# Kernel optimization log

Hardware: AMD Instinct MI355X
Metric: run time of the kernel (lower is better)

The kernel has to match this reference:

```python
import jax, jax.numpy as jnp
import numpy as np


def _shared_mlp(x, W, s, b):
    # 1x1 conv over channel dim (last axis) + folded BN (scale/shift) + ReLU
    # x: (..., Cin), W: (Cout, Cin), s/b: (Cout,)
    return jax.nn.relu(jnp.einsum('...c,oc->...o', x, W) * s + b)


def setup_inputs() -> dict:
    key = jax.random.key(0)
    ks = jax.random.split(key, 15)
    B, N, K, C = 4, 4096, 32, 64
    D1, D2, DH = 64, 64, 128
    sc = 0.1
    return {
        'xyz': jax.random.normal(ks[0], (B, N, 3), dtype=jnp.float32),
        'features': jax.random.normal(ks[1], (B, C, N), dtype=jnp.float32),
        'idx': jax.random.randint(ks[2], (N, K), 0, N, dtype=jnp.int32),
        'W_gu': jax.random.normal(ks[3], (D1, 6), dtype=jnp.float32) * sc,
        's_gu': jnp.ones((D1,), jnp.float32),
        'b_gu': jax.random.normal(ks[4], (D1,), dtype=jnp.float32) * sc,
        'W_gv': jax.random.normal(ks[5], (D2, C), dtype=jnp.float32) * sc,
        's_gv': jnp.ones((D2,), jnp.float32),
        'b_gv': jax.random.normal(ks[6], (D2,), dtype=jnp.float32) * sc,
        'W_h': jax.random.normal(ks[7], (DH, D1 + D2), dtype=jnp.float32) * sc,
        's_h': jnp.ones((DH,), jnp.float32),
        'b_h': jax.random.normal(ks[8], (DH,), dtype=jnp.float32) * sc,
        'W_f': jax.random.normal(ks[9], (C, DH), dtype=jnp.float32) * sc,
        's_f': jnp.ones((C,), jnp.float32),
        'b_f': jax.random.normal(ks[10], (C,), dtype=jnp.float32) * sc,
    }


def reference(xyz, features, idx, W_gu, s_gu, b_gu, W_gv, s_gv, b_gv,
              W_h, s_h, b_h, W_f, s_f, b_f):
    # xyz: (B,N,3), features: (B,C,N), idx: (N,K) neighbor indices per point
    feats = jnp.swapaxes(features, 1, 2)              # (B,N,C)
    xyz_nb = xyz[:, idx, :]                           # (B,N,K,3) random gather
    feat_nb = feats[:, idx, :]                        # (B,N,K,C)
    K = idx.shape[1]
    center_xyz = jnp.broadcast_to(xyz[:, :, None, :], xyz_nb.shape)
    rel_xyz = jnp.concatenate([center_xyz, xyz_nb], axis=-1)   # (B,N,K,6)
    rel_feat = feat_nb + feats[:, :, None, :]                  # (B,N,K,C)

    gu = _shared_mlp(rel_xyz, W_gu, s_gu, b_gu)       # (B,N,K,D1)
    gv = _shared_mlp(rel_feat, W_gv, s_gv, b_gv)      # (B,N,K,D2)
    fuse = jnp.concatenate([gu, gv], axis=-1)         # (B,N,K,D1+D2)
    h = _shared_mlp(fuse, W_h, s_h, b_h)              # (B,N,K,DH)
    pooled = jnp.mean(h, axis=2)                      # (B,N,DH) mean over K
    out = _shared_mlp(pooled, W_f, s_f, b_f)          # (B,N,C)
    out = jnp.swapaxes(out, 1, 2) + features          # (B,C,N) residual
    return (xyz, out)
```

## Files before the change

kernel.cpp:

```cpp
#include <hip/hip_runtime.h>

#define B_  4
#define N_  4096
#define K_  32
#define C_  64
#define DH_ 128
#define PPB 16

typedef _Float16 half2v __attribute__((ext_vector_type(2)));
typedef _Float16 half8  __attribute__((ext_vector_type(8)));
typedef __fp16   fp16x2 __attribute__((ext_vector_type(2)));
typedef float  floatx16 __attribute__((ext_vector_type(16)));
typedef unsigned int uint_t;

union HU { half2v h; uint_t u; };
union HU2 { fp16x2 h; uint_t u; };

__device__ __forceinline__ uint_t pk2(float a, float b) {
    HU2 x; x.h = __builtin_amdgcn_cvt_pkrtz(a, b);
    return x.u;
}

__global__ __launch_bounds__(256) void k_prep(
    const float* __restrict__ xyz,
    const float* __restrict__ features,
    const float* __restrict__ W_gv,
    const float* __restrict__ W_gu,
    const float* __restrict__ s_gu, const float* __restrict__ b_gu,
    const float* __restrict__ s_gv, const float* __restrict__ b_gv,
    const float* __restrict__ W_h,  const float* __restrict__ s_h,
    float* __restrict__ out_xyz,
    _Float16* __restrict__ Bpack,
    uint_t* __restrict__ QsH,
    uint_t* __restrict__ PcatH)
{
    const int blk = blockIdx.x;
    const int b   = blk >> 7;
    const int n0  = (blk & 127) * 32;
    const int t   = threadIdx.x;

    if (t < 96) { int e = blk*96 + t; out_xyz[e] = xyz[e]; }
    {
        int e = blk*32 + t;
        if (t < 32) {
            int j = e & 7, l = (e >> 3) & 63, c = (e >> 9) & 7, ob = e >> 12;
            int o = ob*32 + (l & 31);
            int i = c*16 + (l >> 5)*8 + j;
            Bpack[e] = (_Float16)(W_h[o*DH_ + i] * s_h[o]);
        }
    }

    __shared__ __align__(16) float ftile[64 * 33];
    __shared__ __align__(16) float wtile[64 * 68];

#pragma unroll
    for (int r = 0; r < 2; r++) {
        const int i4 = r*256 + t, c = i4 >> 3, nq = i4 & 7;
        const float4 f4 = *(const float4*)&features[(b*C_ + c)*N_ + n0 + nq*4];
        ftile[c*33 + nq*4 + 0] = f4.x;
        ftile[c*33 + nq*4 + 1] = f4.y;
        ftile[c*33 + nq*4 + 2] = f4.z;
        ftile[c*33 + nq*4 + 3] = f4.w;
    }
#pragma unroll
    for (int r = 0; r < 4; r++) {
        const int e4 = r*256 + t, o = e4 >> 4, c0 = (e4 & 15)*4;
        const float4 w4 = *(const float4*)&W_gv[o*C_ + c0];
        wtile[(c0+0)*68 + o] = w4.x;
        wtile[(c0+1)*68 + o] = w4.y;
        wtile[(c0+2)*68 + o] = w4.z;
        wtile[(c0+3)*68 + o] = w4.w;
    }
    __syncthreads();

    const int n  = t >> 3;
    const int og = t & 7;
    const int o0 = og * 8;

    float acc[8] = {};
    for (int c = 0; c < 64; c++) {
        const float a = ftile[c*33 + n];
        float wv[8];
        *(float4*)&wv[0] = *(const float4*)&wtile[c*68 + o0];
        *(float4*)&wv[4] = *(const float4*)&wtile[c*68 + o0 + 4];
#pragma unroll
        for (int oo = 0; oo < 8; oo++)
            acc[oo] = fmaf(a, wv[oo], acc[oo]);
    }

    const int bn = b*N_ + n0 + n;
    const float x0 = xyz[bn*3+0], x1 = xyz[bn*3+1], x2 = xyz[bn*3+2];

    float sgu[8], bgu[8], sgv[8], bgv[8];
    *(float4*)&sgu[0] = *(const float4*)&s_gu[o0]; *(float4*)&sgu[4] = *(const float4*)&s_gu[o0+4];
    *(float4*)&bgu[0] = *(const float4*)&b_gu[o0]; *(float4*)&bgu[4] = *(const float4*)&b_gu[o0+4];
    *(float4*)&sgv[0] = *(const float4*)&s_gv[o0]; *(float4*)&sgv[4] = *(const float4*)&s_gv[o0+4];
    *(float4*)&bgv[0] = *(const float4*)&b_gv[o0]; *(float4*)&bgv[4] = *(const float4*)&b_gv[o0+4];

    float qv[8], rv[8];
#pragma unroll
    for (int oo = 0; oo < 8; oo++) {
        const int o = o0 + oo;
        qv[oo] = x0*W_gu[o*6+0] + x1*W_gu[o*6+1] + x2*W_gu[o*6+2];
        rv[oo] = x0*W_gu[o*6+3] + x1*W_gu[o*6+4] + x2*W_gu[o*6+5];
    }
    uint4 qa, pa;
    qa.x = pk2(qv[0]*sgu[0]+bgu[0], qv[1]*sgu[1]+bgu[1]);
    qa.y = pk2(qv[2]*sgu[2]+bgu[2], qv[3]*sgu[3]+bgu[3]);
    qa.z = pk2(qv[4]*sgu[4]+bgu[4], qv[5]*sgu[5]+bgu[5]);
    qa.w = pk2(qv[6]*sgu[6]+bgu[6], qv[7]*sgu[7]+bgu[7]);
    pa.x = pk2(rv[0]*sgu[0], rv[1]*sgu[1]);
    pa.y = pk2(rv[2]*sgu[2], rv[3]*sgu[3]);
    pa.z = pk2(rv[4]*sgu[4], rv[5]*sgu[5]);
    pa.w = pk2(rv[6]*sgu[6], rv[7]*sgu[7]);
    *(uint4*)&QsH  [bn*64 + og*4] = qa;
    *(uint4*)&PcatH[bn*64 + og*4] = pa;
    qa.x = pk2(acc[0]*sgv[0]+bgv[0], acc[1]*sgv[1]+bgv[1]);
    qa.y = pk2(acc[2]*sgv[2]+bgv[2], acc[3]*sgv[3]+bgv[3]);
    qa.z = pk2(acc[4]*sgv[4]+bgv[4], acc[5]*sgv[5]+bgv[5]);
    qa.w = pk2(acc[6]*sgv[6]+bgv[6], acc[7]*sgv[7]+bgv[7]);
    pa.x = pk2(acc[0]*sgv[0], acc[1]*sgv[1]);
    pa.y = pk2(acc[2]*sgv[2], acc[3]*sgv[3]);
    pa.z = pk2(acc[4]*sgv[4], acc[5]*sgv[5]);
    pa.w = pk2(acc[6]*sgv[6], acc[7]*sgv[7]);
    *(uint4*)&QsH  [bn*64 + 32 + og*4] = qa;
    *(uint4*)&PcatH[bn*64 + 32 + og*4] = pa;
}

__global__ __launch_bounds__(256) void k_main(
    const int*      __restrict__ idx,
    const uint_t*   __restrict__ QsH,
    const uint_t*   __restrict__ PcatH,
    const _Float16* __restrict__ Bpack,
    const float*    __restrict__ b_h,
    const float*    __restrict__ W_f,
    const float*    __restrict__ s_f, const float* __restrict__ b_f,
    const float*    __restrict__ features,
    float* __restrict__ outF)
{
    const int t    = threadIdx.x;
    const int w    = t >> 6;
    const int lane = t & 63;
    const int m    = lane & 31;
    const int hh   = lane >> 5;
    const int slot = w >> 1;
    const int oh   = w & 1;

    __shared__ uint_t fuse[2 * 32 * 66];
    __shared__ __align__(16) float pooledAll[PPB * 132];

    half8 Bf[2][8];
#pragma unroll
    for (int ob = 0; ob < 2; ob++)
#pragma unroll
        for (int c = 0; c < 8; c++)
            Bf[ob][c] = *(const half8*)&Bpack[(((oh*2 + ob)*8 + c)*64 + lane)*8];

    const float bh0 = b_h[(oh*2+0)*32 + m];
    const float bh1 = b_h[(oh*2+1)*32 + m];

    const int bnb   = blockIdx.x * PPB;
    const int base0 = bnb & ~(N_ - 1);
    const half2v zero2 = {(_Float16)0.f, (_Float16)0.f};

    int jallv[PPB/2];
#pragma unroll
    for (int r = 0; r < PPB/2; r++)
        jallv[r] = idx[((bnb + r*2 + hh) & (N_-1))*K_ + m];

    uint_t qw0 = QsH[(bnb+0)*64 + lane];
    uint_t qw1 = QsH[(bnb+1)*64 + lane];
    uint_t pg[16];
#pragma unroll
    for (int it = 0; it < 16; it++) {
        const int rs = it*4 + w;
        const int j  = __shfl(jallv[0], rs);
        pg[it] = PcatH[(size_t)(base0 + j)*64 + lane];
    }

#pragma unroll
    for (int rr = 0; rr < PPB/2; rr++) {
#pragma unroll
        for (int it = 0; it < 16; it++) {
            const int rs  = it*4 + w;
            const int sl  = rs >> 5, row = rs & 31;
            HU a, p; a.u = sl ? qw1 : qw0; p.u = pg[it];
            half2v v = a.h + p.h;
            v = __builtin_elementwise_max(v, zero2);
            HU o2; o2.h = v;
            fuse[sl*2112 + row*66 + lane] = o2.u;
        }
        if (rr + 1 < PPB/2) {
            const int bn0n = bnb + (rr+1)*2;
            qw0 = QsH[(bn0n+0)*64 + lane];
            qw1 = QsH[(bn0n+1)*64 + lane];
#pragma unroll
            for (int it = 0; it < 16; it++) {
                const int rs = it*4 + w;
                const int j  = __shfl(jallv[rr+1], rs);
                pg[it] = PcatH[(size_t)(base0 + j)*64 + lane];
            }
        }
        __syncthreads();

        floatx16 acc0 = {}, acc1 = {};
#pragma unroll
        for (int c = 0; c < 8; c++) {
            const int wb = slot*2112 + m*66 + c*8 + hh*4;
            union { uint_t u[4]; half8 h; } av;
            *(uint2*)&av.u[0] = *(const uint2*)&fuse[wb];
            *(uint2*)&av.u[2] = *(const uint2*)&fuse[wb + 2];
            acc0 = __builtin_amdgcn_mfma_f32_32x32x16_f16(av.h, Bf[0][c], acc0, 0, 0, 0);
            acc1 = __builtin_amdgcn_mfma_f32_32x32x16_f16(av.h, Bf[1][c], acc1, 0, 0, 0);
        }

        float v0 = 0.f, v1 = 0.f;
#pragma unroll
        for (int rg = 0; rg < 16; rg++) {
            v0 += fmaxf(acc0[rg] + bh0, 0.f);
            v1 += fmaxf(acc1[rg] + bh1, 0.f);
        }
        v0 += __shfl_xor(v0, 32);
        v1 += __shfl_xor(v1, 32);
        const int nl = rr*2 + slot;
        if (hh == 0) {
            pooledAll[nl*132 + (oh*2+0)*32 + m] = v0;
            pooledAll[nl*132 + (oh*2+1)*32 + m] = v1;
        }
        __syncthreads();
    }

    const int b  = bnb >> 12;
    const int n0 = bnb & (N_ - 1);
    const int c  = t >> 2;
    const int nq = t & 3;

    float acc[4] = {};
    for (int i0 = 0; i0 < DH_; i0 += 4) {
        const float4 wv = *(const float4*)&W_f[c*DH_ + i0];
#pragma unroll
        for (int r = 0; r < 4; r++) {
            const float4 p = *(const float4*)&pooledAll[(nq*4 + r)*132 + i0];
            acc[r] += wv.x*p.x + wv.y*p.y + wv.z*p.z + wv.w*p.w;
        }
    }
    const float sfc = s_f[c] * (1.f/(float)K_);
    const float bfc = b_f[c];
    const float4 fr = *(const float4*)&features[(b*C_ + c)*N_ + n0 + nq*4];
    float4 ov;
    ov.x = fmaxf(acc[0]*sfc + bfc, 0.f) + fr.x;
    ov.y = fmaxf(acc[1]*sfc + bfc, 0.f) + fr.y;
    ov.z = fmaxf(acc[2]*sfc + bfc, 0.f) + fr.z;
    ov.w = fmaxf(acc[3]*sfc + bfc, 0.f) + fr.w;
    *(float4*)&outF[(b*C_ + c)*N_ + n0 + nq*4] = ov;
}

extern "C" void kernel_launch(void* const* d_in, const int* in_sizes, int n_in,
                              void* d_out, int out_size, void* d_ws, size_t ws_size,
                              hipStream_t stream)
{
    const float* xyz      = (const float*)d_in[0];
    const float* features = (const float*)d_in[1];
    const int*   idx      = (const int*)  d_in[2];
    const float* W_gu     = (const float*)d_in[3];
    const float* s_gu     = (const float*)d_in[4];
    const float* b_gu     = (const float*)d_in[5];
    const float* W_gv     = (const float*)d_in[6];
    const float* s_gv     = (const float*)d_in[7];
    const float* b_gv     = (const float*)d_in[8];
    const float* W_h      = (const float*)d_in[9];
    const float* s_h      = (const float*)d_in[10];
    const float* b_h      = (const float*)d_in[11];
    const float* W_f      = (const float*)d_in[12];
    const float* s_f      = (const float*)d_in[13];
    const float* b_f      = (const float*)d_in[14];

    float* out  = (float*)d_out;
    float* outF = out + B_*N_*3;

    char* wp = (char*)d_ws;
    uint_t*   QsH   = (uint_t*)wp;   wp += (size_t)B_*N_*64*4;
    uint_t*   PcatH = (uint_t*)wp;   wp += (size_t)B_*N_*64*4;
    _Float16* Bpack = (_Float16*)wp; wp += DH_*DH_*2;

    k_prep<<<B_*(N_/32), 256, 0, stream>>>(xyz, features, W_gv, W_gu,
                                           s_gu, b_gu, s_gv, b_gv, W_h, s_h,
                                           out, Bpack, QsH, PcatH);
    k_main<<<(B_*N_)/PPB, 256, 0, stream>>>(idx, QsH, PcatH, Bpack, b_h,
                                            W_f, s_f, b_f, features, outF);
}
```

Baseline: 130.4 us.

## Fuse prep and main kernels with grid-wide atomic barrier and per-wave point processing

Merges the two kernels into one persistent launch of 512 blocks. A global atomic counter acts as a grid barrier between the precompute phase and the gather/MFMA phase. The main phase now gives each wave its own 8 points, computing all 128 output channels per wave and dropping the block-level __syncthreads between points. The bias add is folded into a max against the negated bias plus 32*bias. This removes one launch gap and intra-block syncs, but adds a memset, a spin barrier that relies on all blocks being co-resident, and larger register use for Bf[4][8] and pg[32].

```diff
diff --git a/kernel.cpp b/kernel.cpp
--- a/kernel.cpp
+++ b/kernel.cpp
@@ -5,7 +5,8 @@
 #define K_  32
 #define C_  64
 #define DH_ 128
-#define PPB 16
+#define PPW 8
+#define NBLK 512
 
 typedef _Float16 half2v __attribute__((ext_vector_type(2)));
 typedef _Float16 half8  __attribute__((ext_vector_type(8)));
@@ -21,238 +22,270 @@
     return x.u;
 }
 
-__global__ __launch_bounds__(256) void k_prep(
+__global__ __launch_bounds__(256, 2) void k_fused(
     const float* __restrict__ xyz,
     const float* __restrict__ features,
+    const int*   __restrict__ idx,
     const float* __restrict__ W_gv,
     const float* __restrict__ W_gu,
     const float* __restrict__ s_gu, const float* __restrict__ b_gu,
     const float* __restrict__ s_gv, const float* __restrict__ b_gv,
     const float* __restrict__ W_h,  const float* __restrict__ s_h,
+    const float* __restrict__ b_h,
+    const float* __restrict__ W_f,
+    const float* __restrict__ s_f,  const float* __restrict__ b_f,
     float* __restrict__ out_xyz,
     _Float16* __restrict__ Bpack,
     uint_t* __restrict__ QsH,
-    uint_t* __restrict__ PcatH)
+    uint_t* __restrict__ PcatH,
+    uint_t* __restrict__ ctr,
+    float* __restrict__ outF)
 {
+    __shared__ __align__(16) uint_t sh[8448];
+    const int t   = threadIdx.x;
     const int blk = blockIdx.x;
-    const int b   = blk >> 7;
-    const int n0  = (blk & 127) * 32;
-    const int t   = threadIdx.x;
-
-    if (t < 96) { int e = blk*96 + t; out_xyz[e] = xyz[e]; }
+
     {
-        int e = blk*32 + t;
-        if (t < 32) {
+        const int b  = blk >> 7;
+        const int n0 = (blk & 127) * 32;
+        float* ftile = (float*)sh;
+        float* wtile = (float*)sh + 64*33;
+
+        if (t < 96) { int e = blk*96 + t; out_xyz[e] = xyz[e]; }
+        if (t >= 128 && t < 160) {
+            int e = blk*32 + (t - 128);
             int j = e & 7, l = (e >> 3) & 63, c = (e >> 9) & 7, ob = e >> 12;
             int o = ob*32 + (l & 31);
             int i = c*16 + (l >> 5)*8 + j;
             Bpack[e] = (_Float16)(W_h[o*DH_ + i] * s_h[o]);
         }
-    }
-
-    __shared__ __align__(16) float ftile[64 * 33];
-    __shared__ __align__(16) float wtile[64 * 68];
-
-#pragma unroll
-    for (int r = 0; r < 2; r++) {
-        const int i4 = r*256 + t, c = i4 >> 3, nq = i4 & 7;
-        const float4 f4 = *(const float4*)&features[(b*C_ + c)*N_ + n0 + nq*4];
-        ftile[c*33 + nq*4 + 0] = f4.x;
-        ftile[c*33 + nq*4 + 1] = f4.y;
-        ftile[c*33 + nq*4 + 2] = f4.z;
-        ftile[c*33 + nq*4 + 3] = f4.w;
-    }
-#pragma unroll
-    for (int r = 0; r < 4; r++) {
-        const int e4 = r*256 + t, o = e4 >> 4, c0 = (e4 & 15)*4;
-        const float4 w4 = *(const float4*)&W_gv[o*C_ + c0];
-        wtile[(c0+0)*68 + o] = w4.x;
-        wtile[(c0+1)*68 + o] = w4.y;
-        wtile[(c0+2)*68 + o] = w4.z;
-        wtile[(c0+3)*68 + o] = w4.w;
-    }
+
+#pragma unroll
+        for (int r = 0; r < 2; r++) {
+            const int i4 = r*256 + t, c = i4 >> 3, nq = i4 & 7;
+            const float4 f4 = *(const float4*)&features[(b*C_ + c)*N_ + n0 + nq*4];
+            ftile[c*33 + nq*4 + 0] = f4.x;
+            ftile[c*33 + nq*4 + 1] = f4.y;
+            ftile[c*33 + nq*4 + 2] = f4.z;
+            ftile[c*33 + nq*4 + 3] = f4.w;
+        }
+#pragma unroll
+        for (int r = 0; r < 4; r++) {
+            const int e4 = r*256 + t, o = e4 >> 4, c0 = (e4 & 15)*4;
+            const float4 w4 = *(const float4*)&W_gv[o*C_ + c0];
+            wtile[(c0+0)*68 + o] = w4.x;
+            wtile[(c0+1)*68 + o] = w4.y;
+            wtile[(c0+2)*68 + o] = w4.z;
+            wtile[(c0+3)*68 + o] = w4.w;
+        }
+        __syncthreads();
+
+        const int n  = t >> 3;
+        const int og = t & 7;
+        const int o0 = og * 8;
+
+        float acc[8] = {};
+        for (int c = 0; c < 64; c++) {
+            const float a = ftile[c*33 + n];
+            float wv[8];
+            *(float4*)&wv[0] = *(const float4*)&wtile[c*68 + o0];
+            *(float4*)&wv[4] = *(const float4*)&wtile[c*68 + o0 + 4];
+#pragma unroll
+            for (int oo = 0; oo < 8; oo++)
+                acc[oo] = fmaf(a, wv[oo], acc[oo]);
+        }
+
+        const int bn = b*N_ + n0 + n;
+        const float x0 = xyz[bn*3+0], x1 = xyz[bn*3+1], x2 = xyz[bn*3+2];
+
+        float sgu[8], bgu[8], sgv[8], bgv[8];
+        *(float4*)&sgu[0] = *(const float4*)&s_gu[o0]; *(float4*)&sgu[4] = *(const float4*)&s_gu[o0+4];
+        *(float4*)&bgu[0] = *(const float4*)&b_gu[o0]; *(float4*)&bgu[4] = *(const float4*)&b_gu[o0+4];
+        *(float4*)&sgv[0] = *(const float4*)&s_gv[o0]; *(float4*)&sgv[4] = *(const float4*)&s_gv[o0+4];
+        *(float4*)&bgv[0] = *(const float4*)&b_gv[o0]; *(float4*)&bgv[4] = *(const float4*)&b_gv[o0+4];
+
+        float qv[8], rv[8];
+#pragma unroll
+        for (int oo = 0; oo < 8; oo++) {
+            const int o = o0 + oo;
+            qv[oo] = x0*W_gu[o*6+0] + x1*W_gu[o*6+1] + x2*W_gu[o*6+2];
+            rv[oo] = x0*W_gu[o*6+3] + x1*W_gu[o*6+4] + x2*W_gu[o*6+5];
+        }
+        uint4 qa, pa;
+        qa.x = pk2(qv[0]*sgu[0]+bgu[0], qv[1]*sgu[1]+bgu[1]);
+        qa.y = pk2(qv[2]*sgu[2]+bgu[2], qv[3]*sgu[3]+bgu[3]);
+        qa.z = pk2(qv[4]*sgu[4]+bgu[4], qv[5]*sgu[5]+bgu[5]);
+        qa.w = pk2(qv[6]*sgu[6]+bgu[6], qv[7]*sgu[7]+bgu[7]);
+        pa.x = pk2(rv[0]*sgu[0], rv[1]*sgu[1]);
+        pa.y = pk2(rv[2]*sgu[2], rv[3]*sgu[3]);
+        pa.z = pk2(rv[4]*sgu[4], rv[5]*sgu[5]);
+        pa.w = pk2(rv[6]*sgu[6], rv[7]*sgu[7]);
+        *(uint4*)&QsH  [bn*64 + og*4] = qa;
+        *(uint4*)&PcatH[bn*64 + og*4] = pa;
+        qa.x = pk2(acc[0]*sgv[0]+bgv[0], acc[1]*sgv[1]+bgv[1]);
+        qa.y = pk2(acc[2]*sgv[2]+bgv[2], acc[3]*sgv[3]+bgv[3]);
+        qa.z = pk2(acc[4]*sgv[4]+bgv[4], acc[5]*sgv[5]+bgv[5]);
+        qa.w = pk2(acc[6]*sgv[6]+bgv[6], acc[7]*sgv[7]+bgv[7]);
+        pa.x = pk2(acc[0]*sgv[0], acc[1]*sgv[1]);
+        pa.y = pk2(acc[2]*sgv[2], acc[3]*sgv[3]);
+        pa.z = pk2(acc[4]*sgv[4], acc[5]*sgv[5]);
+        pa.w = pk2(acc[6]*sgv[6], acc[7]*sgv[7]);
+        *(uint4*)&QsH  [bn*64 + 32 + og*4] = qa;
+        *(uint4*)&PcatH[bn*64 + 32 + og*4] = pa;
+    }
+
     __syncthreads();
-
-    const int n  = t >> 3;
-    const int og = t & 7;
-    const int o0 = og * 8;
-
-    float acc[8] = {};
-    for (int c = 0; c < 64; c++) {
-        const float a = ftile[c*33 + n];
-        float wv[8];
-        *(float4*)&wv[0] = *(const float4*)&wtile[c*68 + o0];
-        *(float4*)&wv[4] = *(const float4*)&wtile[c*68 + o0 + 4];
-#pragma unroll
-        for (int oo = 0; oo < 8; oo++)
-            acc[oo] = fmaf(a, wv[oo], acc[oo]);
-    }
-
-    const int bn = b*N_ + n0 + n;
-    const float x0 = xyz[bn*3+0], x1 = xyz[bn*3+1], x2 = xyz[bn*3+2];
-
-    float sgu[8], bgu[8], sgv[8], bgv[8];
-    *(float4*)&sgu[0] = *(const float4*)&s_gu[o0]; *(float4*)&sgu[4] = *(const float4*)&s_gu[o0+4];
-    *(float4*)&bgu[0] = *(const float4*)&b_gu[o0]; *(float4*)&bgu[4] = *(const float4*)&b_gu[o0+4];
-    *(float4*)&sgv[0] = *(const float4*)&s_gv[o0]; *(float4*)&sgv[4] = *(const float4*)&s_gv[o0+4];
-    *(float4*)&bgv[0] = *(const float4*)&b_gv[o0]; *(float4*)&bgv[4] = *(const float4*)&b_gv[o0+4];
-
-    float qv[8], rv[8];
-#pragma unroll
-    for (int oo = 0; oo < 8; oo++) {
-        const int o = o0 + oo;
-        qv[oo] = x0*W_gu[o*6+0] + x1*W_gu[o*6+1] + x2*W_gu[o*6+2];
-        rv[oo] = x0*W_gu[o*6+3] + x1*W_gu[o*6+4] + x2*W_gu[o*6+5];
-    }
-    uint4 qa, pa;
-    qa.x = pk2(qv[0]*sgu[0]+bgu[0], qv[1]*sgu[1]+bgu[1]);
-    qa.y = pk2(qv[2]*sgu[2]+bgu[2], qv[3]*sgu[3]+bgu[3]);
-    qa.z = pk2(qv[4]*sgu[4]+bgu[4], qv[5]*sgu[5]+bgu[5]);
-    qa.w = pk2(qv[6]*sgu[6]+bgu[6], qv[7]*sgu[7]+bgu[7]);
-    pa.x = pk2(rv[0]*sgu[0], rv[1]*sgu[1]);
-    pa.y = pk2(rv[2]*sgu[2], rv[3]*sgu[3]);
-    pa.z = pk2(rv[4]*sgu[4], rv[5]*sgu[5]);
-    pa.w = pk2(rv[6]*sgu[6], rv[7]*sgu[7]);
-    *(uint4*)&QsH  [bn*64 + og*4] = qa;
-    *(uint4*)&PcatH[bn*64 + og*4] = pa;
-    qa.x = pk2(acc[0]*sgv[0]+bgv[0], acc[1]*sgv[1]+bgv[1]);
-    qa.y = pk2(acc[2]*sgv[2]+bgv[2], acc[3]*sgv[3]+bgv[3]);
-    qa.z = pk2(acc[4]*sgv[4]+bgv[4], acc[5]*sgv[5]+bgv[5]);
-    qa.w = pk2(acc[6]*sgv[6]+bgv[6], acc[7]*sgv[7]+bgv[7]);
-    pa.x = pk2(acc[0]*sgv[0], acc[1]*sgv[1]);
-    pa.y = pk2(acc[2]*sgv[2], acc[3]*sgv[3]);
-    pa.z = pk2(acc[4]*sgv[4], acc[5]*sgv[5]);
-    pa.w = pk2(acc[6]*sgv[6], acc[7]*sgv[7]);
-    *(uint4*)&QsH  [bn*64 + 32 + og*4] = qa;
-    *(uint4*)&PcatH[bn*64 + 32 + og*4] = pa;
-}
-
-__global__ __launch_bounds__(256) void k_main(
-    const int*      __restrict__ idx,
-    const uint_t*   __restrict__ QsH,
-    const uint_t*   __restrict__ PcatH,
-    const _Float16* __restrict__ Bpack,
-    const float*    __restrict__ b_h,
-    const float*    __restrict__ W_f,
-    const float*    __restrict__ s_f, const float* __restrict__ b_f,
-    const float*    __restrict__ features,
-    float* __restrict__ outF)
-{
-    const int t    = threadIdx.x;
-    const int w    = t >> 6;
+    if (t == 0) {
+        __threadfence();
+        atomicAdd(ctr, 1u);
+        while (__hip_atomic_load(ctr, __ATOMIC_RELAXED,
+                                 __HIP_MEMORY_SCOPE_AGENT) < (uint_t)NBLK)
+            __builtin_amdgcn_s_sleep(2);
+    }
+    __syncthreads();
+    __threadfence();
+
+    const int wq   = __builtin_amdgcn_readfirstlane(t >> 6);
     const int lane = t & 63;
     const int m    = lane & 31;
     const int hh   = lane >> 5;
-    const int slot = w >> 1;
-    const int oh   = w & 1;
-
-    __shared__ uint_t fuse[2 * 32 * 66];
-    __shared__ __align__(16) float pooledAll[PPB * 132];
-
-    half8 Bf[2][8];
-#pragma unroll
-    for (int ob = 0; ob < 2; ob++)
+    uint_t* fuse = sh + wq*2112;
+
+    half8 Bf[4][8];
+#pragma unroll
+    for (int ob = 0; ob < 4; ob++)
 #pragma unroll
         for (int c = 0; c < 8; c++)
-            Bf[ob][c] = *(const half8*)&Bpack[(((oh*2 + ob)*8 + c)*64 + lane)*8];
-
-    const float bh0 = b_h[(oh*2+0)*32 + m];
-    const float bh1 = b_h[(oh*2+1)*32 + m];
-
-    const int bnb   = blockIdx.x * PPB;
+            Bf[ob][c] = *(const half8*)&Bpack[((ob*8 + c)*64 + lane)*8];
+
+    float nbh[4], b32[4];
+#pragma unroll
+    for (int ob = 0; ob < 4; ob++) {
+        const float bh = b_h[ob*32 + m];
+        nbh[ob] = -bh;
+        b32[ob] = 32.f * bh;
+    }
+
+    const int gw    = blk*4 + wq;
+    const int bnb   = gw * PPW;
     const int base0 = bnb & ~(N_ - 1);
-    const half2v zero2 = {(_Float16)0.f, (_Float16)0.f};
-
-    int jallv[PPB/2];
-#pragma unroll
-    for (int r = 0; r < PPB/2; r++)
-        jallv[r] = idx[((bnb + r*2 + hh) & (N_-1))*K_ + m];
-
-    uint_t qw0 = QsH[(bnb+0)*64 + lane];
-    uint_t qw1 = QsH[(bnb+1)*64 + lane];
-    uint_t pg[16];
-#pragma unroll
-    for (int it = 0; it < 16; it++) {
-        const int rs = it*4 + w;
-        const int j  = __shfl(jallv[0], rs);
-        pg[it] = PcatH[(size_t)(base0 + j)*64 + lane];
-    }
-
-#pragma unroll
-    for (int rr = 0; rr < PPB/2; rr++) {
-#pragma unroll
-        for (int it = 0; it < 16; it++) {
-            const int rs  = it*4 + w;
-            const int sl  = rs >> 5, row = rs & 31;
-            HU a, p; a.u = sl ? qw1 : qw0; p.u = pg[it];
-            half2v v = a.h + p.h;
-            v = __builtin_elementwise_max(v, zero2);
-            HU o2; o2.h = v;
-            fuse[sl*2112 + row*66 + lane] = o2.u;
-        }
-        if (rr + 1 < PPB/2) {
-            const int bn0n = bnb + (rr+1)*2;
-            qw0 = QsH[(bn0n+0)*64 + lane];
-            qw1 = QsH[(bn0n+1)*64 + lane];
-#pragma unroll
-            for (int it = 0; it < 16; it++) {
-                const int rs = it*4 + w;
-                const int j  = __shfl(jallv[rr+1], rs);
-                pg[it] = PcatH[(size_t)(base0 + j)*64 + lane];
-            }
-        }
-        __syncthreads();
-
-        floatx16 acc0 = {}, acc1 = {};
+
+    uint_t pg[32];
+    uint_t qw;
+    float  pool_r[PPW][4];
+
+    {
+        const int* ip = idx + (bnb & (N_-1))*K_;
+        int js[32];
+#pragma unroll
+        for (int it = 0; it < 32; it++) js[it] = ip[it];
+        qw = QsH[(size_t)bnb*64 + lane];
+#pragma unroll
+        for (int it = 0; it < 32; it++)
+            pg[it] = PcatH[((size_t)(base0 + js[it]) << 6) + lane];
+#pragma unroll
+        for (int it = 0; it < 32; it++) {
+            HU a, pv; a.u = qw; pv.u = pg[it];
+            half2v v = a.h + pv.h;
+            HU o2; o2.h = __builtin_elementwise_max(v, (half2v){(_Float16)0.f,(_Float16)0.f});
+            fuse[it*66 + lane] = o2.u;
+        }
+    }
+
+#pragma unroll
+    for (int p = 0; p < PPW; p++) {
+        uint_t qw_n = 0;
+        if (p + 1 < PPW) {
+            const int* ip = idx + ((bnb + p + 1) & (N_-1))*K_;
+            int js[32];
+#pragma unroll
+            for (int it = 0; it < 32; it++) js[it] = ip[it];
+            qw_n = QsH[(size_t)(bnb + p + 1)*64 + lane];
+#pragma unroll
+            for (int it = 0; it < 32; it++)
+                pg[it] = PcatH[((size_t)(base0 + js[it]) << 6) + lane];
+        }
+
+        floatx16 acc0 = {}, acc1 = {}, acc2 = {}, acc3 = {};
 #pragma unroll
         for (int c = 0; c < 8; c++) {
-            const int wb = slot*2112 + m*66 + c*8 + hh*4;
+            const int wb = m*66 + c*8 + hh*4;
             union { uint_t u[4]; half8 h; } av;
             *(uint2*)&av.u[0] = *(const uint2*)&fuse[wb];
             *(uint2*)&av.u[2] = *(const uint2*)&fuse[wb + 2];
             acc0 = __builtin_amdgcn_mfma_f32_32x32x16_f16(av.h, Bf[0][c], acc0, 0, 0, 0);
             acc1 = __builtin_amdgcn_mfma_f32_32x32x16_f16(av.h, Bf[1][c], acc1, 0, 0, 0);
-        }
-
-        float v0 = 0.f, v1 = 0.f;
+            acc2 = __builtin_amdgcn_mfma_f32_32x32x16_f16(av.h, Bf[2][c], acc2, 0, 0, 0);
+            acc3 = __builtin_amdgcn_mfma_f32_32x32x16_f16(av.h, Bf[3][c], acc3, 0, 0, 0);
+        }
+
+        float v0 = 0.f, v1 = 0.f, v2 = 0.f, v3 = 0.f;
 #pragma unroll
         for (int rg = 0; rg < 16; rg++) {
-            v0 += fmaxf(acc0[rg] + bh0, 0.f);
-            v1 += fmaxf(acc1[rg] + bh1, 0.f);
+            v0 += fmaxf(acc0[rg], nbh[0]);
+            v1 += fmaxf(acc1[rg], nbh[1]);
+            v2 += fmaxf(acc2[rg], nbh[2]);
+            v3 += fmaxf(acc3[rg], nbh[3]);
         }
         v0 += __shfl_xor(v0, 32);
         v1 += __shfl_xor(v1, 32);
-        const int nl = rr*2 + slot;
-        if (hh == 0) {
-            pooledAll[nl*132 + (oh*2+0)*32 + m] = v0;
-            pooledAll[nl*132 + (oh*2+1)*32 + m] = v1;
-        }
-        __syncthreads();
+        v2 += __shfl_xor(v2, 32);
+        v3 += __shfl_xor(v3, 32);
+        pool_r[p][0] = v0 + b32[0];
+        pool_r[p][1] = v1 + b32[1];
+        pool_r[p][2] = v2 + b32[2];
+        pool_r[p][3] = v3 + b32[3];
+
+        if (p + 1 < PPW) {
+#pragma unroll
+            for (int it = 0; it < 32; it++) {
+                HU a, pv; a.u = qw_n; pv.u = pg[it];
+                half2v v = a.h + pv.h;
+                HU o2; o2.h = __builtin_elementwise_max(v, (half2v){(_Float16)0.f,(_Float16)0.f});
+                fuse[it*66 + lane] = o2.u;
+            }
+        }
+    }
+
+    float* poolL = (float*)fuse;
+    if (hh == 0) {
+#pragma unroll
+        for (int p = 0; p < PPW; p++) {
+            poolL[p*132 +  0 + m] = pool_r[p][0];
+            poolL[p*132 + 32 + m] = pool_r[p][1];
+            poolL[p*132 + 64 + m] = pool_r[p][2];
+            poolL[p*132 + 96 + m] = pool_r[p][3];
+        }
     }
 
     const int b  = bnb >> 12;
     const int n0 = bnb & (N_ - 1);
-    const int c  = t >> 2;
-    const int nq = t & 3;
-
-    float acc[4] = {};
+    const int c  = lane;
+
+    float accf[PPW] = {};
     for (int i0 = 0; i0 < DH_; i0 += 4) {
         const float4 wv = *(const float4*)&W_f[c*DH_ + i0];
 #pragma unroll
-        for (int r = 0; r < 4; r++) {
-            const float4 p = *(const float4*)&pooledAll[(nq*4 + r)*132 + i0];
-            acc[r] += wv.x*p.x + wv.y*p.y + wv.z*p.z + wv.w*p.w;
+        for (int p = 0; p < PPW; p++) {
+            const float4 p4 = *(const float4*)&poolL[p*132 + i0];
+            accf[p] += wv.x*p4.x + wv.y*p4.y + wv.z*p4.z + wv.w*p4.w;
         }
     }
     const float sfc = s_f[c] * (1.f/(float)K_);
     const float bfc = b_f[c];
-    const float4 fr = *(const float4*)&features[(b*C_ + c)*N_ + n0 + nq*4];
-    float4 ov;
-    ov.x = fmaxf(acc[0]*sfc + bfc, 0.f) + fr.x;
-    ov.y = fmaxf(acc[1]*sfc + bfc, 0.f) + fr.y;
-    ov.z = fmaxf(acc[2]*sfc + bfc, 0.f) + fr.z;
-    ov.w = fmaxf(acc[3]*sfc + bfc, 0.f) + fr.w;
-    *(float4*)&outF[(b*C_ + c)*N_ + n0 + nq*4] = ov;
+    const float4 fr0 = *(const float4*)&features[(b*C_ + c)*N_ + n0];
+    const float4 fr1 = *(const float4*)&features[(b*C_ + c)*N_ + n0 + 4];
+    float4 ov0, ov1;
+    ov0.x = fmaxf(accf[0]*sfc + bfc, 0.f) + fr0.x;
+    ov0.y = fmaxf(accf[1]*sfc + bfc, 0.f) + fr0.y;
+    ov0.z = fmaxf(accf[2]*sfc + bfc, 0.f) + fr0.z;
+    ov0.w = fmaxf(accf[3]*sfc + bfc, 0.f) + fr0.w;
+    ov1.x = fmaxf(accf[4]*sfc + bfc, 0.f) + fr1.x;
+    ov1.y = fmaxf(accf[5]*sfc + bfc, 0.f) + fr1.y;
+    ov1.z = fmaxf(accf[6]*sfc + bfc, 0.f) + fr1.z;
+    ov1.w = fmaxf(accf[7]*sfc + bfc, 0.f) + fr1.w;
+    *(float4*)&outF[(b*C_ + c)*N_ + n0]     = ov0;
+    *(float4*)&outF[(b*C_ + c)*N_ + n0 + 4] = ov1;
 }
 
 extern "C" void kernel_launch(void* const* d_in, const int* in_sizes, int n_in,
@@ -282,10 +315,11 @@
     uint_t*   QsH   = (uint_t*)wp;   wp += (size_t)B_*N_*64*4;
     uint_t*   PcatH = (uint_t*)wp;   wp += (size_t)B_*N_*64*4;
     _Float16* Bpack = (_Float16*)wp; wp += DH_*DH_*2;
-
-    k_prep<<<B_*(N_/32), 256, 0, stream>>>(xyz, features, W_gv, W_gu,
-                                           s_gu, b_gu, s_gv, b_gv, W_h, s_h,
-                                           out, Bpack, QsH, PcatH);
-    k_main<<<(B_*N_)/PPB, 256, 0, stream>>>(idx, QsH, PcatH, Bpack, b_h,
-                                            W_f, s_f, b_f, features, outF);
+    uint_t*   ctr   = (uint_t*)wp;   wp += 64;
+
+    hipMemsetAsync((void*)ctr, 0, 4, stream);
+    k_fused<<<NBLK, 256, 0, stream>>>(xyz, features, idx, W_gv, W_gu,
+                                      s_gu, b_gu, s_gv, b_gv, W_h, s_h, b_h,
+                                      W_f, s_f, b_f,
+                                      out, Bpack, QsH, PcatH, ctr, outF);
 }
```

After: 188.2 us. 44.3% more time.
